# Optimization experiments

Measured on AMD Instinct MI355X. Metric: run time of the kernel, lower is better.

The kernel has to match this reference:

```python
import jax, jax.numpy as jnp
import numpy as np

N_NODES = 50000
N_EDGES = 800000
IN_CH = 128
OUT_CH = 64
SELF_LOOP_W = 2.0  # improved=True in GCNConv


def setup_inputs() -> dict:
    key = jax.random.key(0)
    k1, k2, k3, k4 = jax.random.split(key, 4)
    x = jax.random.normal(k1, (N_NODES, IN_CH), dtype=jnp.float32)
    edge_index = jax.random.randint(k2, (2, N_EDGES), 0, N_NODES, dtype=jnp.int64)
    edge_weight = jax.random.uniform(k3, (N_EDGES,), dtype=jnp.float32)
    W = jax.random.normal(k4, (IN_CH, OUT_CH), dtype=jnp.float32) / np.sqrt(IN_CH)
    b = jnp.zeros((OUT_CH,), dtype=jnp.float32)
    return {"x": x, "edge_index": edge_index, "edge_weight": edge_weight, "W": W, "b": b}


def reference(x, edge_index, edge_weight, W, b):
    # Only the first GCNConv layer runs (the torch loop returns after k=0).
    N = x.shape[0]
    row, col = edge_index[0], edge_index[1]  # source, target

    # gcn_norm with add_self_loops=True, improved=True (fill value 2.0)
    loop_idx = jnp.arange(N, dtype=edge_index.dtype)
    row_f = jnp.concatenate([row, loop_idx])
    col_f = jnp.concatenate([col, loop_idx])
    ew_f = jnp.concatenate([edge_weight, jnp.full((N,), SELF_LOOP_W, dtype=edge_weight.dtype)])

    deg = jax.ops.segment_sum(ew_f, col_f, num_segments=N)          # [N]
    dinv = jnp.where(deg > 0, jax.lax.rsqrt(deg), 0.0)
    norm = dinv[row_f] * ew_f * dinv[col_f]                          # [E+N]

    # linear transform then normalized sparse aggregation
    xw = x @ W                                                       # [N, out]
    msg = norm[:, None] * xw[row_f]                                  # [E+N, out] gather
    out = jax.ops.segment_sum(msg, col_f, num_segments=N)           # [N, out] scatter-add
    return out + b
```

## Files before the change

kernel.cpp:

```cpp
#include <hip/hip_runtime.h>

constexpr int N    = 50000;
constexpr int E    = 800000;
constexpr int CIN  = 128;
constexpr int COUT = 64;
constexpr float SELF_LOOP_W = 2.0f;

constexpr int NB   = (N + 63) / 64;
constexpr int CAP  = 1536;
constexpr int EPB  = 4096;
constexpr int PBLK = (E + EPB - 1) / EPB;

typedef float vfloat4 __attribute__((ext_vector_type(4)));
typedef int   vint2   __attribute__((ext_vector_type(2)));

__global__ void init_kernel(int* __restrict__ bcur) {
    int i = blockIdx.x * blockDim.x + threadIdx.x;
    if (i < NB) bcur[i] = i * CAP;
}

__global__ __launch_bounds__(512) void partition_kernel(const int* __restrict__ row,
                                                        const int* __restrict__ col,
                                                        const float* __restrict__ ew,
                                                        int* __restrict__ bcur,
                                                        vint2* __restrict__ pk) {
    __shared__ int lhist[NB];
    __shared__ int lbase[NB];
    const int t  = threadIdx.x;
    const int e0 = blockIdx.x * EPB;

    for (int i = t; i < NB; i += 512) lhist[i] = 0;
    __syncthreads();

    #pragma unroll
    for (int k = 0; k < EPB / 512; ++k) {
        int e = e0 + k * 512 + t;
        if (e < E) atomicAdd(&lhist[col[e] >> 6], 1);
    }
    __syncthreads();

    for (int i = t; i < NB; i += 512) {
        int h = lhist[i];
        lbase[i] = (h > 0) ? atomicAdd(&bcur[i], h) : 0;
    }
    __syncthreads();
    for (int i = t; i < NB; i += 512) lhist[i] = 0;
    __syncthreads();

    #pragma unroll
    for (int k = 0; k < EPB / 512; ++k) {
        int e = e0 + k * 512 + t;
        if (e < E) {
            int c   = col[e];
            int bkt = c >> 6;
            int p = lbase[bkt] + atomicAdd(&lhist[bkt], 1);
            if (p < (bkt + 1) * CAP) {
                vint2 v;
                v.x = row[e] | ((c & 63) << 20);
                v.y = __float_as_int(ew[e]);
                pk[p] = v;
            }
        }
    }
}

__global__ __launch_bounds__(256) void deg_kernel(const int* __restrict__ bcur,
                                                  const vint2* __restrict__ pk,
                                                  float* __restrict__ dinv) {
    __shared__ float ldeg[64];
    const int t    = threadIdx.x;
    const int b    = blockIdx.x;
    const int base = b * CAP;
    const int cnt  = min(bcur[b] - base, CAP);

    if (t < 64) ldeg[t] = 0.f;
    __syncthreads();
    for (int j = t; j < cnt; j += 256) {
        vint2 v = pk[base + j];
        atomicAdd(&ldeg[(v.x >> 20) & 63], __int_as_float(v.y));
    }
    __syncthreads();
    int node = b * 64 + t;
    if (t < 64 && node < N) dinv[node] = rsqrtf(SELF_LOOP_W + ldeg[t]);
}

__global__ __launch_bounds__(256) void xw_kernel(const float* __restrict__ x,
                                                 const float* __restrict__ W,
                                                 float* __restrict__ xw) {
    __shared__ __align__(16) float xs[64][132];

    const int t    = threadIdx.x;
    const int base = blockIdx.x * 64;

    #pragma unroll
    for (int i = 0; i < 8; ++i) {
        int f4  = i * 256 + t;
        int r   = f4 >> 5;
        int c4  = f4 & 31;
        int node = base + r;
        if (node >= N) node = N - 1;
        vfloat4 v = *(const vfloat4*)(x + (size_t)node * CIN + c4 * 4);
        *(vfloat4*)&xs[r][c4 * 4] = v;
    }
    __syncthreads();

    const int tc = t & 15;
    const int tn = t >> 4;

    float acc[4][4];
    #pragma unroll
    for (int i = 0; i < 4; ++i)
        #pragma unroll
        for (int j = 0; j < 4; ++j) acc[i][j] = 0.f;

    const float* Wp = W + tc * 4;
    #pragma unroll 8
    for (int k = 0; k < CIN; ++k) {
        vfloat4 bv = *(const vfloat4*)(Wp + (size_t)k * COUT);
        float a0 = xs[tn * 4 + 0][k];
        float a1 = xs[tn * 4 + 1][k];
        float a2 = xs[tn * 4 + 2][k];
        float a3 = xs[tn * 4 + 3][k];
        #pragma unroll
        for (int j = 0; j < 4; ++j) {
            acc[0][j] += a0 * bv[j];
            acc[1][j] += a1 * bv[j];
            acc[2][j] += a2 * bv[j];
            acc[3][j] += a3 * bv[j];
        }
    }

    #pragma unroll
    for (int i = 0; i < 4; ++i) {
        int node = base + tn * 4 + i;
        if (node >= N) continue;
        vfloat4 xv;
        #pragma unroll
        for (int j = 0; j < 4; ++j) xv[j] = acc[i][j];
        *(vfloat4*)(xw + (size_t)node * COUT + tc * 4) = xv;
    }
}

__global__ __launch_bounds__(512) void aggregate_kernel(const int* __restrict__ bcur,
                                                        const vint2* __restrict__ pk,
                                                        const float* __restrict__ dinv,
                                                        const float* __restrict__ xw,
                                                        const float* __restrict__ bias,
                                                        float* __restrict__ out) {
    __shared__ int   s_r[CAP];
    __shared__ float s_n[CAP];
    __shared__ int   lhist[64], lofs[64], lcur[64];

    const int t    = threadIdx.x;
    const int lane = t & 63;
    const int wv   = t >> 6;
    const int b    = blockIdx.x;
    const int base = b * CAP;
    const int cnt  = min(bcur[b] - base, CAP);

    if (t < 64) lhist[t] = 0;
    __syncthreads();

    for (int j = t; j < cnt; j += 512)
        atomicAdd(&lhist[(pk[base + j].x >> 20) & 63], 1);
    __syncthreads();

    if (t < 64) {
        int v = lhist[t];
        int s = v;
        #pragma unroll
        for (int d = 1; d < 64; d <<= 1) {
            int u = __shfl_up(s, d);
            if (lane >= d) s += u;
        }
        lofs[t] = s - v;
        lcur[t] = s - v;
    }
    __syncthreads();

    for (int j = t; j < cnt; j += 512) {
        vint2 v = pk[base + j];
        int   r  = v.x & 0xFFFFF;
        int   ln = (v.x >> 20) & 63;
        float n  = __int_as_float(v.y) * dinv[r];
        int   p  = atomicAdd(&lcur[ln], 1);
        s_r[p] = r;
        s_n[p] = n;
    }
    __syncthreads();

    float bl = bias[lane];
    for (int nd = wv; nd < 64; nd += 8) {
        int node = b * 64 + nd;
        if (node >= N) continue;
        int s0 = lofs[nd];
        int e0 = s0 + lhist[nd];
        float acc = 0.f;
        int i = s0;
        for (; i + 4 <= e0; i += 4) {
            int   r0 = s_r[i],     r1 = s_r[i + 1], r2 = s_r[i + 2], r3 = s_r[i + 3];
            float n0 = s_n[i],     n1 = s_n[i + 1], n2 = s_n[i + 2], n3 = s_n[i + 3];
            float v0 = xw[(size_t)r0 * COUT + lane];
            float v1 = xw[(size_t)r1 * COUT + lane];
            float v2 = xw[(size_t)r2 * COUT + lane];
            float v3 = xw[(size_t)r3 * COUT + lane];
            acc += n0 * v0; acc += n1 * v1; acc += n2 * v2; acc += n3 * v3;
        }
        for (; i < e0; ++i)
            acc += s_n[i] * xw[(size_t)s_r[i] * COUT + lane];

        float dc = dinv[node];
        float xv = xw[(size_t)node * COUT + lane];
        out[(size_t)node * COUT + lane] =
            dc * acc + SELF_LOOP_W * dc * dc * xv + bl;
    }
}

extern "C" void kernel_launch(void* const* d_in, const int* in_sizes, int n_in,
                              void* d_out, int out_size, void* d_ws, size_t ws_size,
                              hipStream_t stream) {
    const float* x  = (const float*)d_in[0];
    const int*   ei = (const int*)d_in[1];
    const float* ew = (const float*)d_in[2];
    const float* W  = (const float*)d_in[3];
    const float* b  = (const float*)d_in[4];
    float* out = (float*)d_out;

    float* xw   = (float*)d_ws;
    float* dinv = xw + (size_t)N * COUT;
    int*   bcur = (int*)(dinv + N);
    vint2* pk   = (vint2*)(bcur + NB);

    const int* rowp = ei;
    const int* colp = ei + E;

    init_kernel     <<<(NB + 255) / 256, 256, 0, stream>>>(bcur);
    partition_kernel<<<PBLK, 512, 0, stream>>>(rowp, colp, ew, bcur, pk);
    xw_kernel       <<<NB, 256, 0, stream>>>(x, W, xw);
    deg_kernel      <<<NB, 256, 0, stream>>>(bcur, pk, dinv);
    aggregate_kernel<<<NB, 512, 0, stream>>>(bcur, pk, dinv, xw, b, out);
}
```

Measured before the change: 155.6 us.

## Gather neighbor features from a bf16 copy of XW and stage edges in LDS

The xw kernel now also writes a bf16 copy of the transformed features, and the aggregation gathers neighbor rows from that copy. This halves the bytes of the dominant random gather. The aggregate kernel also caches the packed edges and their normalized weights in shared memory on the first pass, so the global loads and dinv lookups are not repeated, and it unrolls the gather loop to 8. The cost is reduced precision in the aggregated messages, more shared memory per block, which may cut occupancy, and an extra bf16 store in the xw kernel.

Result: no change. 153.2 us (-1.6%).

```diff
diff --git a/kernel.cpp b/kernel.cpp
--- a/kernel.cpp
+++ b/kernel.cpp
@@ -11,8 +11,18 @@
 constexpr int EPB  = 4096;
 constexpr int PBLK = (E + EPB - 1) / EPB;
 
-typedef float vfloat4 __attribute__((ext_vector_type(4)));
-typedef int   vint2   __attribute__((ext_vector_type(2)));
+typedef float          vfloat4  __attribute__((ext_vector_type(4)));
+typedef int            vint2    __attribute__((ext_vector_type(2)));
+typedef unsigned short vushort4 __attribute__((ext_vector_type(4)));
+
+__device__ __forceinline__ unsigned short f2bf(float f) {
+    unsigned int u = __float_as_uint(f);
+    u += 0x7FFFu + ((u >> 16) & 1u);
+    return (unsigned short)(u >> 16);
+}
+__device__ __forceinline__ float bf2f(unsigned short h) {
+    return __uint_as_float(((unsigned int)h) << 16);
+}
 
 __global__ void init_kernel(int* __restrict__ bcur) {
     int i = blockIdx.x * blockDim.x + threadIdx.x;
@@ -86,7 +96,8 @@
 
 __global__ __launch_bounds__(256) void xw_kernel(const float* __restrict__ x,
                                                  const float* __restrict__ W,
-                                                 float* __restrict__ xw) {
+                                                 float* __restrict__ xw,
+                                                 unsigned short* __restrict__ xwh) {
     __shared__ __align__(16) float xs[64][132];
 
     const int t    = threadIdx.x;
@@ -135,9 +146,11 @@
         int node = base + tn * 4 + i;
         if (node >= N) continue;
         vfloat4 xv;
-        #pragma unroll
-        for (int j = 0; j < 4; ++j) xv[j] = acc[i][j];
-        *(vfloat4*)(xw + (size_t)node * COUT + tc * 4) = xv;
+        vushort4 hv;
+        #pragma unroll
+        for (int j = 0; j < 4; ++j) { xv[j] = acc[i][j]; hv[j] = f2bf(acc[i][j]); }
+        *(vfloat4*) (xw  + (size_t)node * COUT + tc * 4) = xv;
+        *(vushort4*)(xwh + (size_t)node * COUT + tc * 4) = hv;
     }
 }
 
@@ -145,8 +158,11 @@
                                                         const vint2* __restrict__ pk,
                                                         const float* __restrict__ dinv,
                                                         const float* __restrict__ xw,
+                                                        const unsigned short* __restrict__ xwh,
                                                         const float* __restrict__ bias,
                                                         float* __restrict__ out) {
+    __shared__ int   rawx[CAP];
+    __shared__ float rawn[CAP];
     __shared__ int   s_r[CAP];
     __shared__ float s_n[CAP];
     __shared__ int   lhist[64], lofs[64], lcur[64];
@@ -161,8 +177,12 @@
     if (t < 64) lhist[t] = 0;
     __syncthreads();
 
-    for (int j = t; j < cnt; j += 512)
-        atomicAdd(&lhist[(pk[base + j].x >> 20) & 63], 1);
+    for (int j = t; j < cnt; j += 512) {
+        vint2 v = pk[base + j];
+        rawx[j] = v.x;
+        rawn[j] = __int_as_float(v.y) * dinv[v.x & 0xFFFFF];
+        atomicAdd(&lhist[(v.x >> 20) & 63], 1);
+    }
     __syncthreads();
 
     if (t < 64) {
@@ -179,13 +199,10 @@
     __syncthreads();
 
     for (int j = t; j < cnt; j += 512) {
-        vint2 v = pk[base + j];
-        int   r  = v.x & 0xFFFFF;
-        int   ln = (v.x >> 20) & 63;
-        float n  = __int_as_float(v.y) * dinv[r];
-        int   p  = atomicAdd(&lcur[ln], 1);
-        s_r[p] = r;
-        s_n[p] = n;
+        int xv = rawx[j];
+        int p  = atomicAdd(&lcur[(xv >> 20) & 63], 1);
+        s_r[p] = xv & 0xFFFFF;
+        s_n[p] = rawn[j];
     }
     __syncthreads();
 
@@ -197,17 +214,18 @@
         int e0 = s0 + lhist[nd];
         float acc = 0.f;
         int i = s0;
-        for (; i + 4 <= e0; i += 4) {
-            int   r0 = s_r[i],     r1 = s_r[i + 1], r2 = s_r[i + 2], r3 = s_r[i + 3];
-            float n0 = s_n[i],     n1 = s_n[i + 1], n2 = s_n[i + 2], n3 = s_n[i + 3];
-            float v0 = xw[(size_t)r0 * COUT + lane];
-            float v1 = xw[(size_t)r1 * COUT + lane];
-            float v2 = xw[(size_t)r2 * COUT + lane];
-            float v3 = xw[(size_t)r3 * COUT + lane];
-            acc += n0 * v0; acc += n1 * v1; acc += n2 * v2; acc += n3 * v3;
+        for (; i + 8 <= e0; i += 8) {
+            int r[8]; float n[8], v[8];
+            #pragma unroll
+            for (int u = 0; u < 8; ++u) { r[u] = s_r[i + u]; n[u] = s_n[i + u]; }
+            #pragma unroll
+            for (int u = 0; u < 8; ++u)
+                v[u] = bf2f(xwh[(size_t)r[u] * COUT + lane]);
+            #pragma unroll
+            for (int u = 0; u < 8; ++u) acc += n[u] * v[u];
         }
         for (; i < e0; ++i)
-            acc += s_n[i] * xw[(size_t)s_r[i] * COUT + lane];
+            acc += s_n[i] * bf2f(xwh[(size_t)s_r[i] * COUT + lane]);
 
         float dc = dinv[node];
         float xv = xw[(size_t)node * COUT + lane];
@@ -226,17 +244,18 @@
     const float* b  = (const float*)d_in[4];
     float* out = (float*)d_out;
 
-    float* xw   = (float*)d_ws;
-    float* dinv = xw + (size_t)N * COUT;
-    int*   bcur = (int*)(dinv + N);
-    vint2* pk   = (vint2*)(bcur + NB);
+    float*          xw   = (float*)d_ws;
+    float*          dinv = xw + (size_t)N * COUT;
+    int*            bcur = (int*)(dinv + N);
+    vint2*          pk   = (vint2*)(bcur + NB + 2);
+    unsigned short* xwh  = (unsigned short*)(pk + (size_t)NB * CAP);
 
     const int* rowp = ei;
     const int* colp = ei + E;
 
     init_kernel     <<<(NB + 255) / 256, 256, 0, stream>>>(bcur);
     partition_kernel<<<PBLK, 512, 0, stream>>>(rowp, colp, ew, bcur, pk);
-    xw_kernel       <<<NB, 256, 0, stream>>>(x, W, xw);
+    xw_kernel       <<<NB, 256, 0, stream>>>(x, W, xw, xwh);
     deg_kernel      <<<NB, 256, 0, stream>>>(bcur, pk, dinv);
-    aggregate_kernel<<<NB, 512, 0, stream>>>(bcur, pk, dinv, xw, b, out);
-}
+    aggregate_kernel<<<NB, 512, 0, stream>>>(bcur, pk, dinv, xw, xwh, b, out);
+}
```
